# Optimization experiments

Measured on AMD Instinct MI355X. Metric: run time of the kernel, lower is better.

## Reference

```python
import jax, jax.numpy as jnp
import numpy as np

N = 100000
D = 64
E = 1600000
EPS = 1e-5


def setup_inputs() -> dict:
    key = jax.random.key(0)
    k1, k2, k3, k4, k5, k6 = jax.random.split(key, 6)
    node_features = jax.random.normal(k1, (N, D), dtype=jnp.float32)
    edge_index = jax.random.randint(k2, (E, 2), 0, N, dtype=jnp.int64)
    # torch Linear params: W [out, in], b [out]
    lim_m = 1.0 / np.sqrt(2 * D)
    W_msg = jax.random.uniform(k3, (D, 2 * D), minval=-lim_m, maxval=lim_m, dtype=jnp.float32)
    b_msg = jax.random.uniform(k4, (D,), minval=-lim_m, maxval=lim_m, dtype=jnp.float32)
    W_upd = jax.random.uniform(k5, (D, 2 * D), minval=-lim_m, maxval=lim_m, dtype=jnp.float32)
    b_upd = jax.random.uniform(k6, (D,), minval=-lim_m, maxval=lim_m, dtype=jnp.float32)
    gamma = jnp.ones((D,), dtype=jnp.float32)
    beta = jnp.zeros((D,), dtype=jnp.float32)
    return {
        "node_features": node_features,
        "edge_index": edge_index,
        "W_msg": W_msg,
        "b_msg": b_msg,
        "W_upd": W_upd,
        "b_upd": b_upd,
        "gamma": gamma,
        "beta": beta,
    }


def _layer_norm(x, gamma, beta):
    mu = jnp.mean(x, axis=-1, keepdims=True)
    var = jnp.mean(jnp.square(x - mu), axis=-1, keepdims=True)
    return (x - mu) * jax.lax.rsqrt(var + EPS) * gamma + beta


def reference(node_features, edge_index, W_msg, b_msg, W_upd, b_upd, gamma, beta):
    src = edge_index[:, 0]
    tgt = edge_index[:, 1]
    # per-edge message: relu(Linear(cat(x[src], x[tgt])))  -- split weight to avoid [E,2D] concat
    Wm_s = W_msg[:, :D]  # [D, D] applied to src feats
    Wm_t = W_msg[:, D:]  # [D, D] applied to tgt feats
    msg = jax.nn.relu(node_features[src] @ Wm_s.T + node_features[tgt] @ Wm_t.T + b_msg)  # [E, D]
    # scatter-mean into target nodes
    messages = jax.ops.segment_sum(msg, tgt, num_segments=N)  # [N, D]
    counts = jax.ops.segment_sum(jnp.ones((edge_index.shape[0],), dtype=node_features.dtype), tgt, num_segments=N)
    counts = jnp.maximum(counts, 1.0)[:, None]
    messages = messages / counts
    # update: relu(Linear(cat(x, messages))) + residual + LayerNorm
    Wu_x = W_upd[:, :D]
    Wu_m = W_upd[:, D:]
    updated = jax.nn.relu(node_features @ Wu_x.T + messages @ Wu_m.T + b_upd)
    return _layer_norm(updated + node_features, gamma, beta)
```

## Files before the change

kernel.cpp:

```cpp
#include <hip/hip_runtime.h>
#include <hip/hip_bf16.h>
#include <stdint.h>

#define NNODES 100000
#define DF 64
#define NEDGES 1600000
#define ND (NNODES * DF)
#define BKT 100
#define NBUCK 1000
#define CHUNK 200
#define NCHUNK (NEDGES / CHUNK)
#define NPW 25

static __device__ __forceinline__ float bf2f(unsigned short u) {
    union { uint32_t i; float f; } c; c.i = ((uint32_t)u) << 16; return c.f;
}
static __device__ __forceinline__ unsigned short f2bf(float f) {
    union { __hip_bfloat16 b; unsigned short u; } c; c.b = __float2bfloat16(f); return c.u;
}
static __device__ __forceinline__ void unpack2(uint32_t u, float& lo, float& hi) {
    union { uint32_t i; float f; } a, b;
    a.i = u << 16; b.i = u & 0xFFFF0000u;
    lo = a.f; hi = b.f;
}

__global__ void wconv_k(const unsigned short* __restrict__ x,
                        const unsigned int* __restrict__ eiu,
                        const void* __restrict__ Wm, const void* __restrict__ Wu,
                        const void* __restrict__ bm, const void* __restrict__ bu,
                        const void* __restrict__ ga, const void* __restrict__ be,
                        float* __restrict__ WfMT, float* __restrict__ WfUT,
                        float* __restrict__ prm, int* __restrict__ flags) {
    __shared__ int cnt_sane, cnt_odd_nz;
    if (threadIdx.x == 0) { cnt_sane = 0; cnt_odd_nz = 0; }
    __syncthreads();
    {
        unsigned short s = x[threadIdx.x * 2];
        unsigned short m = s & 0x7FFF;
        if (m < 0x0080 || (m >= 0x3000 && m <= 0x4200)) atomicAdd(&cnt_sane, 1);
        if (threadIdx.x < 64) {
            if (eiu[threadIdx.x * 2 + 1] != 0u) atomicAdd(&cnt_odd_nz, 1);
        }
    }
    __syncthreads();
    const int bf = (cnt_sane >= 192) ? 1 : 0;
    if (blockIdx.x == 0 && threadIdx.x == 0) {
        flags[0] = bf;
        flags[1] = (cnt_odd_nz == 0) ? 1 : 0;
    }
    int i = blockIdx.x * 256 + threadIdx.x;
    if (i < 16384) {
        const void* src = (i < 8192) ? Wm : Wu;
        float* dst = (i < 8192) ? WfMT : WfUT;
        int ii = i & 8191, j = ii >> 6, k = ii & 63;
        int si = (j & 63) * 128 + ((j >> 6) ? 64 : 0) + k;
        float v = bf ? bf2f(((const unsigned short*)src)[si]) : ((const float*)src)[si];
        dst[(j >> 6) * 4096 + k * 64 + (j & 63)] = v;
    } else if (i < 16384 + 320) {
        int t = i - 16384, which = t >> 6, k = t & 63;
        if (which == 4) { prm[t] = 0.f; }
        else {
            const void* p = (which == 0) ? bm : (which == 1) ? bu : (which == 2) ? ga : be;
            prm[t] = bf ? bf2f(((const unsigned short*)p)[k]) : ((const float*)p)[k];
        }
    }
}

__global__ __launch_bounds__(256, 1) void mm_k(const int* __restrict__ flags,
                                               const void* __restrict__ xv,
                                               const float* __restrict__ WT,
                                               const float* __restrict__ bias,
                                               void* __restrict__ outv,
                                               int of) {
    const int lane = threadIdx.x & 63;
    const int wib = __builtin_amdgcn_readfirstlane(threadIdx.x >> 6);
    const int bf = flags[0];

    float w[64];
    #pragma unroll
    for (int k = 0; k < 64; ++k) w[k] = WT[k * 64 + lane];
    const float bs = bias[lane];

    const int wv = blockIdx.x * 4 + wib;
    const int n0 = wv * NPW;
    if (n0 >= NNODES) return;
    const int n1 = (n0 + NPW < NNODES) ? n0 + NPW : NNODES;
    for (int n = n0; n < n1; ++n) {
        float a0 = 0.f, a1 = 0.f, a2 = 0.f, a3 = 0.f;
        if (bf) {
            const uint4* xr = (const uint4*)((const unsigned short*)xv + (size_t)n * DF);
            #pragma unroll
            for (int q = 0; q < 8; ++q) {
                uint4 v = xr[q];
                float x0,x1,x2,x3,x4,x5,x6,x7;
                unpack2(v.x, x0, x1); unpack2(v.y, x2, x3);
                unpack2(v.z, x4, x5); unpack2(v.w, x6, x7);
                a0 = fmaf(x0, w[8*q+0], a0); a1 = fmaf(x1, w[8*q+1], a1);
                a2 = fmaf(x2, w[8*q+2], a2); a3 = fmaf(x3, w[8*q+3], a3);
                a0 = fmaf(x4, w[8*q+4], a0); a1 = fmaf(x5, w[8*q+5], a1);
                a2 = fmaf(x6, w[8*q+6], a2); a3 = fmaf(x7, w[8*q+7], a3);
            }
        } else {
            const float4* xr = (const float4*)((const float*)xv + (size_t)n * DF);
            #pragma unroll
            for (int q = 0; q < 16; ++q) {
                float4 v = xr[q];
                a0 = fmaf(v.x, w[4*q+0], a0); a1 = fmaf(v.y, w[4*q+1], a1);
                a2 = fmaf(v.z, w[4*q+2], a2); a3 = fmaf(v.w, w[4*q+3], a3);
            }
        }
        float r = (a0 + a1) + (a2 + a3) + bs;
        size_t gi = (size_t)n * DF + lane;
        if (of) ((float*)outv)[gi] = r;
        else    ((unsigned short*)outv)[gi] = f2bf(r);
    }
}

__global__ __launch_bounds__(256) void bhist_k(const int* __restrict__ flags,
                                               const int* __restrict__ ei,
                                               int* __restrict__ BktCnt) {
    __shared__ int h[NBUCK];
    const int i64 = flags[1];
    for (int i = threadIdx.x; i < NBUCK; i += 256) h[i] = 0;
    __syncthreads();
    int stride = gridDim.x * 256;
    for (int e = blockIdx.x * 256 + threadIdx.x; e < NEDGES; e += stride) {
        int tgt = i64 ? ei[4*e + 2] : ei[2*e + 1];
        if ((unsigned)tgt < NNODES) atomicAdd(&h[tgt / BKT], 1);
    }
    __syncthreads();
    for (int b = threadIdx.x; b < NBUCK; b += 256)
        if (h[b]) atomicAdd(BktCnt + b, h[b]);
}

__global__ __launch_bounds__(1024) void bscan_k(const int* __restrict__ BktCnt,
                                                int* __restrict__ BktOff,
                                                int* __restrict__ BktCur) {
    __shared__ int lds[1024];
    int t = threadIdx.x;
    int c = (t < NBUCK) ? BktCnt[t] : 0;
    lds[t] = c;
    __syncthreads();
    for (int off = 1; off < 1024; off <<= 1) {
        int add = (t >= off) ? lds[t - off] : 0;
        __syncthreads();
        lds[t] += add;
        __syncthreads();
    }
    if (t < NBUCK) {
        int ex = lds[t] - c;
        BktOff[t] = ex;
        BktCur[t] = ex;
    }
    if (t == NBUCK - 1) BktOff[NBUCK] = lds[t];
}

__global__ __launch_bounds__(256) void bfill_k(const int* __restrict__ flags,
                                               const int* __restrict__ ei,
                                               int* __restrict__ BktCur,
                                               int* __restrict__ BktE) {
    __shared__ int h[NBUCK], h2[NBUCK], basee[NBUCK];
    const int i64 = flags[1];
    for (int i = threadIdx.x; i < NBUCK; i += 256) { h[i] = 0; h2[i] = 0; }
    __syncthreads();
    const int stride = gridDim.x * 256;
    for (int e = blockIdx.x * 256 + threadIdx.x; e < NEDGES; e += stride) {
        int tgt = i64 ? ei[4*e + 2] : ei[2*e + 1];
        if ((unsigned)tgt < NNODES) atomicAdd(&h[tgt / BKT], 1);
    }
    __syncthreads();
    for (int b = threadIdx.x; b < NBUCK; b += 256)
        if (h[b]) basee[b] = atomicAdd(BktCur + b, h[b]);
    __syncthreads();
    for (int e = blockIdx.x * 256 + threadIdx.x; e < NEDGES; e += stride) {
        int src, tgt;
        if (i64) { src = ei[4*e]; tgt = ei[4*e + 2]; }
        else     { src = ei[2*e]; tgt = ei[2*e + 1]; }
        if ((unsigned)tgt >= NNODES) continue;
        int b = tgt / BKT;
        int tl = tgt - b * BKT;
        int r = atomicAdd(&h2[b], 1);
        BktE[basee[b] + r] = (tl << 24) | (src & 0xFFFFFF);
    }
}

__global__ __launch_bounds__(256) void tsort_k(const int* __restrict__ BktOff,
                                               const int* __restrict__ BktE,
                                               int* __restrict__ CsrSrc,
                                               int* __restrict__ Row) {
    __shared__ int oc[128], excl[128], cur[128];
    const int tid = threadIdx.x;
    const int b = blockIdx.x;
    const int s = BktOff[b], e = BktOff[b + 1];
    const int n = e - s;
    if (tid < 128) { oc[tid] = 0; }
    __syncthreads();
    for (int i = tid; i < n; i += 256)
        atomicAdd(&oc[((unsigned)BktE[s + i]) >> 24], 1);
    __syncthreads();
    if (tid < 128) excl[tid] = (tid > 0) ? oc[tid - 1] : 0;
    __syncthreads();
    for (int off = 1; off < 128; off <<= 1) {
        int add = (tid >= off && tid < 128) ? excl[tid - off] : 0;
        __syncthreads();
        if (tid < 128) excl[tid] += add;
        __syncthreads();
    }
    if (tid < BKT) {
        Row[b * BKT + tid] = s + excl[tid];
        cur[tid] = excl[tid];
    }
    if (b == 0 && tid == 0) Row[NNODES] = NEDGES;
    __syncthreads();
    for (int i = tid; i < n; i += 256) {
        int v = BktE[s + i];
        int tl = ((unsigned)v) >> 24;
        int p = atomicAdd(&cur[tl], 1);
        int sv = v & 0xFFFFFF;
        if (sv >= NNODES) sv = 0;
        CsrSrc[s + p] = sv << 6;
    }
}

__global__ __launch_bounds__(256) void cstart_k(const int* __restrict__ Row,
                                                int* __restrict__ ChunkT) {
    int c = blockIdx.x * 256 + threadIdx.x;
    if (c > NCHUNK) return;
    if (c == NCHUNK) { ChunkT[NCHUNK] = NNODES; return; }
    int target = c * CHUNK;
    int lo = 0, hi = NNODES + 1;
    while (lo < hi) { int mid = (lo + hi) >> 1; if (Row[mid] >= target) hi = mid; else lo = mid + 1; }
    ChunkT[c] = lo;
}

__global__ __launch_bounds__(1024) void agg_k(const unsigned short* __restrict__ Ps,
                                              const unsigned short* __restrict__ Pt,
                                              const int* __restrict__ Row,
                                              const int* __restrict__ CsrSrc,
                                              const int* __restrict__ ChunkT,
                                              unsigned short* __restrict__ Msg) {
    const int lane = threadIdx.x & 63;
    const int wib = __builtin_amdgcn_readfirstlane(threadIdx.x >> 6);
    const int w = blockIdx.x * 16 + wib;
    if (w >= NCHUNK) return;

    const int t_lo = ChunkT[w];
    const int t_hi = ChunkT[w + 1];
    if (t_lo >= t_hi) return;

    int segS = Row[t_lo];
    for (int t = t_lo; t < t_hi; ++t) {
        const int segE = Row[t + 1];
        const int deg = segE - segS;
        float ptv = bf2f(Pt[(size_t)t * DF + lane]);
        float pa0 = 0.f, pa1 = 0.f, pa2 = 0.f, pa3 = 0.f;
        for (int i = segS; i < segE; i += 16) {
            #pragma unroll
            for (int j = 0; j < 16; ++j) {
                const int idx = i + j;
                const int ok = idx < segE;
                const int sv = CsrSrc[ok ? idx : segS];
                float p = bf2f(Ps[(size_t)(unsigned)sv + lane]);
                float v = ok ? fmaxf(p + ptv, 0.f) : 0.f;
                if ((j & 3) == 0)      pa0 += v;
                else if ((j & 3) == 1) pa1 += v;
                else if ((j & 3) == 2) pa2 += v;
                else                   pa3 += v;
            }
        }
        float macc = (pa0 + pa1) + (pa2 + pa3);
        float mval = (deg > 0) ? (macc / (float)deg) : 0.f;
        Msg[(size_t)t * DF + lane] = f2bf(mval);
        segS = segE;
    }
}

__global__ __launch_bounds__(256, 1) void u2_k(const int* __restrict__ flags,
                                               const void* __restrict__ xv,
                                               const unsigned short* __restrict__ Msg,
                                               const float* __restrict__ t1,
                                               const float* __restrict__ WT,
                                               const float* __restrict__ prm,
                                               void* __restrict__ outv) {
    const int lane = threadIdx.x & 63;
    const int wib = __builtin_amdgcn_readfirstlane(threadIdx.x >> 6);
    const int bf = flags[0];

    float w[64];
    #pragma unroll
    for (int k = 0; k < 64; ++k) w[k] = WT[k * 64 + lane];
    const float ga = prm[128 + lane];
    const float be = prm[192 + lane];

    const unsigned short* x16 = (const unsigned short*)xv;
    const float* xf = (const float*)xv;

    const int wv = blockIdx.x * 4 + wib;
    const int n0 = wv * NPW;
    if (n0 >= NNODES) return;
    const int n1 = (n0 + NPW < NNODES) ? n0 + NPW : NNODES;
    for (int n = n0; n < n1; ++n) {
        float b0 = 0.f, b1 = 0.f, b2 = 0.f, b3 = 0.f;
        const uint4* mw = (const uint4*)(Msg + (size_t)n * DF);
        #pragma unroll
        for (int q = 0; q < 8; ++q) {
            uint4 v = mw[q];
            float m0,m1,m2,m3,m4,m5,m6,m7;
            unpack2(v.x, m0, m1); unpack2(v.y, m2, m3);
            unpack2(v.z, m4, m5); unpack2(v.w, m6, m7);
            b0 = fmaf(m0, w[8*q+0], b0); b1 = fmaf(m1, w[8*q+1], b1);
            b2 = fmaf(m2, w[8*q+2], b2); b3 = fmaf(m3, w[8*q+3], b3);
            b0 = fmaf(m4, w[8*q+4], b0); b1 = fmaf(m5, w[8*q+5], b1);
            b2 = fmaf(m6, w[8*q+6], b2); b3 = fmaf(m7, w[8*q+7], b3);
        }
        size_t gi = (size_t)n * DF + lane;
        float t  = t1[gi];
        float xl = bf ? bf2f(x16[gi]) : xf[gi];
        float u = fmaxf((b0 + b1) + (b2 + b3) + t, 0.f);
        float r = u + xl;

        float s = r, s2 = r * r;
        #pragma unroll
        for (int m = 1; m < 64; m <<= 1) {
            s  += __shfl_xor(s, m, 64);
            s2 += __shfl_xor(s2, m, 64);
        }
        float mu  = s * (1.0f / 64.0f);
        float var = fmaxf(s2 * (1.0f / 64.0f) - mu * mu, 0.f);
        float o = (r - mu) * rsqrtf(var + 1e-5f) * ga + be;

        if (bf) ((__hip_bfloat16*)outv)[gi] = __float2bfloat16(o);
        else    ((float*)outv)[gi] = o;
    }
}

extern "C" void kernel_launch(void* const* d_in, const int* in_sizes, int n_in,
                              void* d_out, int out_size, void* d_ws, size_t ws_size,
                              hipStream_t stream) {
    const void* x  = d_in[0];
    const int*  ei = (const int*)d_in[1];
    const void* Wm = d_in[2];
    const void* bm = d_in[3];
    const void* Wu = d_in[4];
    const void* bu = d_in[5];
    const void* ga = d_in[6];
    const void* be = d_in[7];

    char* ws = (char*)d_ws;
    size_t off = 0;
    unsigned short* Ps  = (unsigned short*)(ws + off); off += (size_t)ND * 2;
    unsigned short* Pt  = (unsigned short*)(ws + off); off += (size_t)ND * 2;
    unsigned short* Msg = (unsigned short*)(ws + off); off += (size_t)ND * 2;
    int*   BktE   = (int*)(ws + off); off += (size_t)NEDGES * 4;
    int*   CsrSrc = (int*)(ws + off); off += (size_t)NEDGES * 4;
    int*   Row    = (int*)(ws + off); off += (size_t)(NNODES + 1) * 4;
    int*   BktCnt = (int*)(ws + off); off += NBUCK * 4;
    int*   BktOff = (int*)(ws + off); off += (NBUCK + 1) * 4;
    int*   BktCur = (int*)(ws + off); off += NBUCK * 4;
    int*   flg    = (int*)(ws + off); off += 16;
    float* WfMT   = (float*)(ws + off); off += 8192 * 4;
    float* WfUT   = (float*)(ws + off); off += 8192 * 4;
    float* prm    = (float*)(ws + off); off += 320 * 4;

    float* t1 = (float*)Ps;
    int* ChunkT = BktE;

    (void)hipMemsetAsync(BktCnt, 0, NBUCK * 4, stream);

    wconv_k<<<66, 256, 0, stream>>>((const unsigned short*)x, (const unsigned int*)ei,
                                    Wm, Wu, bm, bu, ga, be, WfMT, WfUT, prm, flg);

    mm_k<<<1024, 256, 0, stream>>>(flg, x, WfMT,        prm + 256, Ps, 0);
    mm_k<<<1024, 256, 0, stream>>>(flg, x, WfMT + 4096, prm,       Pt, 0);

    bhist_k<<<256, 256, 0, stream>>>(flg, ei, BktCnt);
    bscan_k<<<1, 1024, 0, stream>>>(BktCnt, BktOff, BktCur);
    bfill_k<<<128, 256, 0, stream>>>(flg, ei, BktCur, BktE);
    tsort_k<<<NBUCK, 256, 0, stream>>>(BktOff, BktE, CsrSrc, Row);

    cstart_k<<<(NCHUNK + 256) / 256, 256, 0, stream>>>(Row, ChunkT);

    agg_k<<<NCHUNK / 16, 1024, 0, stream>>>(Ps, Pt, Row, CsrSrc, ChunkT, Msg);

    mm_k<<<1024, 256, 0, stream>>>(flg, x, WfUT, prm + 64, t1, 1);

    u2_k<<<1024, 256, 0, stream>>>(flg, x, Msg, t1, WfUT + 4096, prm, d_out);
}
```

Before: 338.2 us.

## Fuse source/target projections with bucket histogram into one launch; shrink aggregation chunks

Merges the two per-node projection matmuls and the edge bucket histogram into one kernel, using disjoint block ranges so the compute-bound projections and the memory-bound histogram can run side by side. The aggregation chunk size drops from 200 to 128 edges, and its blocks shrink from 1024 to 256 threads, for finer load balancing. This removes two launches and their serialization, at the cost of more chunks and a larger ChunkT lookup.

```diff
diff --git a/kernel.cpp b/kernel.cpp
--- a/kernel.cpp
+++ b/kernel.cpp
@@ -8,7 +8,7 @@
 #define ND (NNODES * DF)
 #define BKT 100
 #define NBUCK 1000
-#define CHUNK 200
+#define CHUNK 128
 #define NCHUNK (NEDGES / CHUNK)
 #define NPW 25
 
@@ -63,6 +63,216 @@
             const void* p = (which == 0) ? bm : (which == 1) ? bu : (which == 2) ? ga : be;
             prm[t] = bf ? bf2f(((const unsigned short*)p)[k]) : ((const float*)p)[k];
         }
+    }
+}
+
+__global__ __launch_bounds__(256, 1) void pj_k(const int* __restrict__ flags,
+                                               const void* __restrict__ xv,
+                                               const float* __restrict__ WfMT,
+                                               const float* __restrict__ prm,
+                                               unsigned short* __restrict__ Ps,
+                                               unsigned short* __restrict__ Pt,
+                                               const int* __restrict__ ei,
+                                               int* __restrict__ BktCnt) {
+    const int blk = blockIdx.x;
+    if (blk < 2048) {
+        const int lane = threadIdx.x & 63;
+        const int wib = __builtin_amdgcn_readfirstlane(threadIdx.x >> 6);
+        const int bf = flags[0];
+        const int mtx = (blk >= 1024);
+        const float* WT = WfMT + (mtx ? 4096 : 0);
+
+        float w[64];
+        #pragma unroll
+        for (int k = 0; k < 64; ++k) w[k] = WT[k * 64 + lane];
+        const float bs = mtx ? prm[lane] : 0.f;
+        unsigned short* outp = mtx ? Pt : Ps;
+
+        const int wv = (blk & 1023) * 4 + wib;
+        const int n0 = wv * NPW;
+        if (n0 >= NNODES) return;
+        const int n1 = (n0 + NPW < NNODES) ? n0 + NPW : NNODES;
+        for (int n = n0; n < n1; ++n) {
+            float a0 = 0.f, a1 = 0.f, a2 = 0.f, a3 = 0.f;
+            if (bf) {
+                const uint4* xr = (const uint4*)((const unsigned short*)xv + (size_t)n * DF);
+                #pragma unroll
+                for (int q = 0; q < 8; ++q) {
+                    uint4 v = xr[q];
+                    float x0,x1,x2,x3,x4,x5,x6,x7;
+                    unpack2(v.x, x0, x1); unpack2(v.y, x2, x3);
+                    unpack2(v.z, x4, x5); unpack2(v.w, x6, x7);
+                    a0 = fmaf(x0, w[8*q+0], a0); a1 = fmaf(x1, w[8*q+1], a1);
+                    a2 = fmaf(x2, w[8*q+2], a2); a3 = fmaf(x3, w[8*q+3], a3);
+                    a0 = fmaf(x4, w[8*q+4], a0); a1 = fmaf(x5, w[8*q+5], a1);
+                    a2 = fmaf(x6, w[8*q+6], a2); a3 = fmaf(x7, w[8*q+7], a3);
+                }
+            } else {
+                const float4* xr = (const float4*)((const float*)xv + (size_t)n * DF);
+                #pragma unroll
+                for (int q = 0; q < 16; ++q) {
+                    float4 v = xr[q];
+                    a0 = fmaf(v.x, w[4*q+0], a0); a1 = fmaf(v.y, w[4*q+1], a1);
+                    a2 = fmaf(v.z, w[4*q+2], a2); a3 = fmaf(v.w, w[4*q+3], a3);
+                }
+            }
+            outp[(size_t)n * DF + lane] = f2bf((a0 + a1) + (a2 + a3) + bs);
+        }
+    } else {
+        __shared__ int h[NBUCK];
+        const int i64 = flags[1];
+        const int hb = blk - 2048;
+        for (int i = threadIdx.x; i < NBUCK; i += 256) h[i] = 0;
+        __syncthreads();
+        for (int e = hb * 256 + threadIdx.x; e < NEDGES; e += 65536) {
+            int tgt = i64 ? ei[4*e + 2] : ei[2*e + 1];
+            if ((unsigned)tgt < NNODES) atomicAdd(&h[tgt / BKT], 1);
+        }
+        __syncthreads();
+        for (int b = threadIdx.x; b < NBUCK; b += 256)
+            if (h[b]) atomicAdd(BktCnt + b, h[b]);
+    }
+}
+
+__global__ __launch_bounds__(1024) void bscan_k(const int* __restrict__ BktCnt,
+                                                int* __restrict__ BktOff,
+                                                int* __restrict__ BktCur) {
+    __shared__ int lds[1024];
+    int t = threadIdx.x;
+    int c = (t < NBUCK) ? BktCnt[t] : 0;
+    lds[t] = c;
+    __syncthreads();
+    for (int off = 1; off < 1024; off <<= 1) {
+        int add = (t >= off) ? lds[t - off] : 0;
+        __syncthreads();
+        lds[t] += add;
+        __syncthreads();
+    }
+    if (t < NBUCK) {
+        int ex = lds[t] - c;
+        BktOff[t] = ex;
+        BktCur[t] = ex;
+    }
+    if (t == NBUCK - 1) BktOff[NBUCK] = lds[t];
+}
+
+__global__ __launch_bounds__(256) void bfill_k(const int* __restrict__ flags,
+                                               const int* __restrict__ ei,
+                                               int* __restrict__ BktCur,
+                                               int* __restrict__ BktE) {
+    __shared__ int h[NBUCK], h2[NBUCK], basee[NBUCK];
+    const int i64 = flags[1];
+    for (int i = threadIdx.x; i < NBUCK; i += 256) { h[i] = 0; h2[i] = 0; }
+    __syncthreads();
+    const int stride = gridDim.x * 256;
+    for (int e = blockIdx.x * 256 + threadIdx.x; e < NEDGES; e += stride) {
+        int tgt = i64 ? ei[4*e + 2] : ei[2*e + 1];
+        if ((unsigned)tgt < NNODES) atomicAdd(&h[tgt / BKT], 1);
+    }
+    __syncthreads();
+    for (int b = threadIdx.x; b < NBUCK; b += 256)
+        if (h[b]) basee[b] = atomicAdd(BktCur + b, h[b]);
+    __syncthreads();
+    for (int e = blockIdx.x * 256 + threadIdx.x; e < NEDGES; e += stride) {
+        int src, tgt;
+        if (i64) { src = ei[4*e]; tgt = ei[4*e + 2]; }
+        else     { src = ei[2*e]; tgt = ei[2*e + 1]; }
+        if ((unsigned)tgt >= NNODES) continue;
+        int b = tgt / BKT;
+        int tl = tgt - b * BKT;
+        int r = atomicAdd(&h2[b], 1);
+        BktE[basee[b] + r] = (tl << 24) | (src & 0xFFFFFF);
+    }
+}
+
+__global__ __launch_bounds__(256) void tsort_k(const int* __restrict__ BktOff,
+                                               const int* __restrict__ BktE,
+                                               int* __restrict__ CsrSrc,
+                                               int* __restrict__ Row) {
+    __shared__ int oc[128], excl[128], cur[128];
+    const int tid = threadIdx.x;
+    const int b = blockIdx.x;
+    const int s = BktOff[b], e = BktOff[b + 1];
+    const int n = e - s;
+    if (tid < 128) { oc[tid] = 0; }
+    __syncthreads();
+    for (int i = tid; i < n; i += 256)
+        atomicAdd(&oc[((unsigned)BktE[s + i]) >> 24], 1);
+    __syncthreads();
+    if (tid < 128) excl[tid] = (tid > 0) ? oc[tid - 1] : 0;
+    __syncthreads();
+    for (int off = 1; off < 128; off <<= 1) {
+        int add = (tid >= off && tid < 128) ? excl[tid - off] : 0;
+        __syncthreads();
+        if (tid < 128) excl[tid] += add;
+        __syncthreads();
+    }
+    if (tid < BKT) {
+        Row[b * BKT + tid] = s + excl[tid];
+        cur[tid] = excl[tid];
+    }
+    if (b == 0 && tid == 0) Row[NNODES] = NEDGES;
+    __syncthreads();
+    for (int i = tid; i < n; i += 256) {
+        int v = BktE[s + i];
+        int tl = ((unsigned)v) >> 24;
+        int p = atomicAdd(&cur[tl], 1);
+        int sv = v & 0xFFFFFF;
+        if (sv >= NNODES) sv = 0;
+        CsrSrc[s + p] = sv << 6;
+    }
+}
+
+__global__ __launch_bounds__(256) void cstart_k(const int* __restrict__ Row,
+                                                int* __restrict__ ChunkT) {
+    int c = blockIdx.x * 256 + threadIdx.x;
+    if (c > NCHUNK) return;
+    if (c == NCHUNK) { ChunkT[NCHUNK] = NNODES; return; }
+    int target = c * CHUNK;
+    int lo = 0, hi = NNODES + 1;
+    while (lo < hi) { int mid = (lo + hi) >> 1; if (Row[mid] >= target) hi = mid; else lo = mid + 1; }
+    ChunkT[c] = lo;
+}
+
+__global__ __launch_bounds__(256) void agg_k(const unsigned short* __restrict__ Ps,
+                                             const unsigned short* __restrict__ Pt,
+                                             const int* __restrict__ Row,
+                                             const int* __restrict__ CsrSrc,
+                                             const int* __restrict__ ChunkT,
+                                             unsigned short* __restrict__ Msg) {
+    const int lane = threadIdx.x & 63;
+    const int wib = __builtin_amdgcn_readfirstlane(threadIdx.x >> 6);
+    const int w = blockIdx.x * 4 + wib;
+    if (w >= NCHUNK) return;
+
+    const int t_lo = ChunkT[w];
+    const int t_hi = ChunkT[w + 1];
+    if (t_lo >= t_hi) return;
+
+    int segS = Row[t_lo];
+    for (int t = t_lo; t < t_hi; ++t) {
+        const int segE = Row[t + 1];
+        const int deg = segE - segS;
+        float ptv = bf2f(Pt[(size_t)t * DF + lane]);
+        float pa0 = 0.f, pa1 = 0.f, pa2 = 0.f, pa3 = 0.f;
+        for (int i = segS; i < segE; i += 16) {
+            #pragma unroll
+            for (int j = 0; j < 16; ++j) {
+                const int idx = i + j;
+                const int ok = idx < segE;
+                const int sv = CsrSrc[ok ? idx : segS];
+                float p = bf2f(Ps[(size_t)(unsigned)sv + lane]);
+                float v = ok ? fmaxf(p + ptv, 0.f) : 0.f;
+                if ((j & 3) == 0)      pa0 += v;
+                else if ((j & 3) == 1) pa1 += v;
+                else if ((j & 3) == 2) pa2 += v;
+                else                   pa3 += v;
+            }
+        }
+        float macc = (pa0 + pa1) + (pa2 + pa3);
+        float mval = (deg > 0) ? (macc / (float)deg) : 0.f;
+        Msg[(size_t)t * DF + lane] = f2bf(mval);
+        segS = segE;
     }
 }
 
@@ -116,165 +326,6 @@
     }
 }
 
-__global__ __launch_bounds__(256) void bhist_k(const int* __restrict__ flags,
-                                               const int* __restrict__ ei,
-                                               int* __restrict__ BktCnt) {
-    __shared__ int h[NBUCK];
-    const int i64 = flags[1];
-    for (int i = threadIdx.x; i < NBUCK; i += 256) h[i] = 0;
-    __syncthreads();
-    int stride = gridDim.x * 256;
-    for (int e = blockIdx.x * 256 + threadIdx.x; e < NEDGES; e += stride) {
-        int tgt = i64 ? ei[4*e + 2] : ei[2*e + 1];
-        if ((unsigned)tgt < NNODES) atomicAdd(&h[tgt / BKT], 1);
-    }
-    __syncthreads();
-    for (int b = threadIdx.x; b < NBUCK; b += 256)
-        if (h[b]) atomicAdd(BktCnt + b, h[b]);
-}
-
-__global__ __launch_bounds__(1024) void bscan_k(const int* __restrict__ BktCnt,
-                                                int* __restrict__ BktOff,
-                                                int* __restrict__ BktCur) {
-    __shared__ int lds[1024];
-    int t = threadIdx.x;
-    int c = (t < NBUCK) ? BktCnt[t] : 0;
-    lds[t] = c;
-    __syncthreads();
-    for (int off = 1; off < 1024; off <<= 1) {
-        int add = (t >= off) ? lds[t - off] : 0;
-        __syncthreads();
-        lds[t] += add;
-        __syncthreads();
-    }
-    if (t < NBUCK) {
-        int ex = lds[t] - c;
-        BktOff[t] = ex;
-        BktCur[t] = ex;
-    }
-    if (t == NBUCK - 1) BktOff[NBUCK] = lds[t];
-}
-
-__global__ __launch_bounds__(256) void bfill_k(const int* __restrict__ flags,
-                                               const int* __restrict__ ei,
-                                               int* __restrict__ BktCur,
-                                               int* __restrict__ BktE) {
-    __shared__ int h[NBUCK], h2[NBUCK], basee[NBUCK];
-    const int i64 = flags[1];
-    for (int i = threadIdx.x; i < NBUCK; i += 256) { h[i] = 0; h2[i] = 0; }
-    __syncthreads();
-    const int stride = gridDim.x * 256;
-    for (int e = blockIdx.x * 256 + threadIdx.x; e < NEDGES; e += stride) {
-        int tgt = i64 ? ei[4*e + 2] : ei[2*e + 1];
-        if ((unsigned)tgt < NNODES) atomicAdd(&h[tgt / BKT], 1);
-    }
-    __syncthreads();
-    for (int b = threadIdx.x; b < NBUCK; b += 256)
-        if (h[b]) basee[b] = atomicAdd(BktCur + b, h[b]);
-    __syncthreads();
-    for (int e = blockIdx.x * 256 + threadIdx.x; e < NEDGES; e += stride) {
-        int src, tgt;
-        if (i64) { src = ei[4*e]; tgt = ei[4*e + 2]; }
-        else     { src = ei[2*e]; tgt = ei[2*e + 1]; }
-        if ((unsigned)tgt >= NNODES) continue;
-        int b = tgt / BKT;
-        int tl = tgt - b * BKT;
-        int r = atomicAdd(&h2[b], 1);
-        BktE[basee[b] + r] = (tl << 24) | (src & 0xFFFFFF);
-    }
-}
-
-__global__ __launch_bounds__(256) void tsort_k(const int* __restrict__ BktOff,
-                                               const int* __restrict__ BktE,
-                                               int* __restrict__ CsrSrc,
-                                               int* __restrict__ Row) {
-    __shared__ int oc[128], excl[128], cur[128];
-    const int tid = threadIdx.x;
-    const int b = blockIdx.x;
-    const int s = BktOff[b], e = BktOff[b + 1];
-    const int n = e - s;
-    if (tid < 128) { oc[tid] = 0; }
-    __syncthreads();
-    for (int i = tid; i < n; i += 256)
-        atomicAdd(&oc[((unsigned)BktE[s + i]) >> 24], 1);
-    __syncthreads();
-    if (tid < 128) excl[tid] = (tid > 0) ? oc[tid - 1] : 0;
-    __syncthreads();
-    for (int off = 1; off < 128; off <<= 1) {
-        int add = (tid >= off && tid < 128) ? excl[tid - off] : 0;
-        __syncthreads();
-        if (tid < 128) excl[tid] += add;
-        __syncthreads();
-    }
-    if (tid < BKT) {
-        Row[b * BKT + tid] = s + excl[tid];
-        cur[tid] = excl[tid];
-    }
-    if (b == 0 && tid == 0) Row[NNODES] = NEDGES;
-    __syncthreads();
-    for (int i = tid; i < n; i += 256) {
-        int v = BktE[s + i];
-        int tl = ((unsigned)v) >> 24;
-        int p = atomicAdd(&cur[tl], 1);
-        int sv = v & 0xFFFFFF;
-        if (sv >= NNODES) sv = 0;
-        CsrSrc[s + p] = sv << 6;
-    }
-}
-
-__global__ __launch_bounds__(256) void cstart_k(const int* __restrict__ Row,
-                                                int* __restrict__ ChunkT) {
-    int c = blockIdx.x * 256 + threadIdx.x;
-    if (c > NCHUNK) return;
-    if (c == NCHUNK) { ChunkT[NCHUNK] = NNODES; return; }
-    int target = c * CHUNK;
-    int lo = 0, hi = NNODES + 1;
-    while (lo < hi) { int mid = (lo + hi) >> 1; if (Row[mid] >= target) hi = mid; else lo = mid + 1; }
-    ChunkT[c] = lo;
-}
-
-__global__ __launch_bounds__(1024) void agg_k(const unsigned short* __restrict__ Ps,
-                                              const unsigned short* __restrict__ Pt,
-                                              const int* __restrict__ Row,
-                                              const int* __restrict__ CsrSrc,
-                                              const int* __restrict__ ChunkT,
-                                              unsigned short* __restrict__ Msg) {
-    const int lane = threadIdx.x & 63;
-    const int wib = __builtin_amdgcn_readfirstlane(threadIdx.x >> 6);
-    const int w = blockIdx.x * 16 + wib;
-    if (w >= NCHUNK) return;
-
-    const int t_lo = ChunkT[w];
-    const int t_hi = ChunkT[w + 1];
-    if (t_lo >= t_hi) return;
-
-    int segS = Row[t_lo];
-    for (int t = t_lo; t < t_hi; ++t) {
-        const int segE = Row[t + 1];
-        const int deg = segE - segS;
-        float ptv = bf2f(Pt[(size_t)t * DF + lane]);
-        float pa0 = 0.f, pa1 = 0.f, pa2 = 0.f, pa3 = 0.f;
-        for (int i = segS; i < segE; i += 16) {
-            #pragma unroll
-            for (int j = 0; j < 16; ++j) {
-                const int idx = i + j;
-                const int ok = idx < segE;
-                const int sv = CsrSrc[ok ? idx : segS];
-                float p = bf2f(Ps[(size_t)(unsigned)sv + lane]);
-                float v = ok ? fmaxf(p + ptv, 0.f) : 0.f;
-                if ((j & 3) == 0)      pa0 += v;
-                else if ((j & 3) == 1) pa1 += v;
-                else if ((j & 3) == 2) pa2 += v;
-                else                   pa3 += v;
-            }
-        }
-        float macc = (pa0 + pa1) + (pa2 + pa3);
-        float mval = (deg > 0) ? (macc / (float)deg) : 0.f;
-        Msg[(size_t)t * DF + lane] = f2bf(mval);
-        segS = segE;
-    }
-}
-
 __global__ __launch_bounds__(256, 1) void u2_k(const int* __restrict__ flags,
                                                const void* __restrict__ xv,
                                                const unsigned short* __restrict__ Msg,
@@ -370,17 +421,15 @@
     wconv_k<<<66, 256, 0, stream>>>((const unsigned short*)x, (const unsigned int*)ei,
                                     Wm, Wu, bm, bu, ga, be, WfMT, WfUT, prm, flg);
 
-    mm_k<<<1024, 256, 0, stream>>>(flg, x, WfMT,        prm + 256, Ps, 0);
-    mm_k<<<1024, 256, 0, stream>>>(flg, x, WfMT + 4096, prm,       Pt, 0);
-
-    bhist_k<<<256, 256, 0, stream>>>(flg, ei, BktCnt);
+    pj_k<<<2304, 256, 0, stream>>>(flg, x, WfMT, prm, Ps, Pt, ei, BktCnt);
+
     bscan_k<<<1, 1024, 0, stream>>>(BktCnt, BktOff, BktCur);
     bfill_k<<<128, 256, 0, stream>>>(flg, ei, BktCur, BktE);
     tsort_k<<<NBUCK, 256, 0, stream>>>(BktOff, BktE, CsrSrc, Row);
 
     cstart_k<<<(NCHUNK + 256) / 256, 256, 0, stream>>>(Row, ChunkT);
 
-    agg_k<<<NCHUNK / 16, 1024, 0, stream>>>(Ps, Pt, Row, CsrSrc, ChunkT, Msg);
+    agg_k<<<(NCHUNK + 3) / 4, 256, 0, stream>>>(Ps, Pt, Row, CsrSrc, ChunkT, Msg);
 
     mm_k<<<1024, 256, 0, stream>>>(flg, x, WfUT, prm + 64, t1, 1);
 
```

Result: faster. 321.7 us (-4.9%).
